# Kernel optimization log

Measured on AMD Instinct MI355X. Metric: run time of the kernel, lower is better.

The kernel has to match this reference:

```python
import jax, jax.numpy as jnp
import numpy as np

NEG_SLOPE = 0.2
EPS = 1e-16


def _add_self_loops(edge_index, num_nodes):
    loop = jnp.arange(num_nodes, dtype=edge_index.dtype)
    return jnp.concatenate([edge_index, jnp.stack([loop, loop])], axis=1)


def gat_conv(x, edge_index, W, a_src, a_dst, b, concat):
    """PyG-style GATConv: gather -> attention logits -> segment softmax -> scatter-add."""
    N = x.shape[0]
    H, C = a_src.shape
    xl = (x @ W).reshape(N, H, C)                       # [N,H,C]
    alpha_src = (xl * a_src[None]).sum(-1)              # [N,H]
    alpha_dst = (xl * a_dst[None]).sum(-1)              # [N,H]
    src, dst = edge_index[0], edge_index[1]
    alpha = jax.nn.leaky_relu(alpha_src[src] + alpha_dst[dst], NEG_SLOPE)  # [E,H]
    amax = jax.ops.segment_max(alpha, dst, num_segments=N)
    amax = jnp.where(jnp.isfinite(amax), amax, 0.0)
    ea = jnp.exp(alpha - amax[dst])
    denom = jax.ops.segment_sum(ea, dst, num_segments=N)
    attn = ea / (denom[dst] + EPS)                      # [E,H]
    msg = xl[src] * attn[:, :, None]                    # [E,H,C]
    out = jax.ops.segment_sum(msg, dst, num_segments=N)  # [N,H,C]
    out = out.reshape(N, H * C) if concat else out.mean(axis=1)
    return out + b


def setup_inputs() -> dict:
    key = jax.random.key(0)
    ks = jax.random.split(key, 9)
    N, F, E, H, C, NC = 100000, 128, 1600000, 8, 8, 40
    s = lambda fan: 1.0 / np.sqrt(fan)
    return {
        "x": jax.random.normal(ks[0], (N, F), dtype=jnp.float32),
        "edge_index": jax.random.randint(ks[1], (2, E), 0, N, dtype=jnp.int64),
        "W1": jax.random.normal(ks[2], (F, H * C), dtype=jnp.float32) * s(F),
        "a_src1": jax.random.normal(ks[3], (H, C), dtype=jnp.float32) * s(C),
        "a_dst1": jax.random.normal(ks[4], (H, C), dtype=jnp.float32) * s(C),
        "b1": jnp.zeros((H * C,), dtype=jnp.float32),
        "W2": jax.random.normal(ks[5], (H * C, NC), dtype=jnp.float32) * s(H * C),
        "a_src2": jax.random.normal(ks[6], (1, NC), dtype=jnp.float32) * s(NC),
        "a_dst2": jax.random.normal(ks[7], (1, NC), dtype=jnp.float32) * s(NC),
        "b2": jnp.zeros((NC,), dtype=jnp.float32),
    }


def reference(x, edge_index, W1, a_src1, a_dst1, b1, W2, a_src2, a_dst2, b2):
    N = x.shape[0]
    ei = _add_self_loops(edge_index, N)
    h = gat_conv(x, ei, W1, a_src1, a_dst1, b1, concat=True)   # [N,64]
    h = jax.nn.elu(h)
    out = gat_conv(h, ei, W2, a_src2, a_dst2, b2, concat=True)  # [N,nclass]
    return out
```

## Files before the change

kernel.cpp:

```cpp
#include <hip/hip_runtime.h>
#include <math.h>

#define NEG_SLOPE 0.2f
#define GAT_EPS 1e-16f

#define CH   8192
#define NBK  256

__device__ __forceinline__ unsigned pack_bf16(float a, float b) {
    unsigned ua = __float_as_uint(a);
    unsigned ub = __float_as_uint(b);
    ua = (ua + 0x8000u) >> 16;
    ub = (ub + 0x8000u) & 0xffff0000u;
    return ua | ub;
}
__device__ __forceinline__ float bf_lo(unsigned pk) {
    return __uint_as_float(pk << 16);
}
__device__ __forceinline__ float bf_hi(unsigned pk) {
    return __uint_as_float(pk & 0xffff0000u);
}


__global__ __launch_bounds__(256) void k_cnt(
    const int* __restrict__ ei, int E, int N, int shift,
    int* __restrict__ cnt)
{
    __shared__ int h[NBK];
    int c = blockIdx.x;
    h[threadIdx.x] = 0;
    __syncthreads();
    int Etot = E + N;
    int base = c * CH;
    int lim = min(base + CH, Etot);
    for (int e = base + threadIdx.x; e < lim; e += 256) {
        int d = (e < E) ? ei[E + e] : (e - E);
        atomicAdd(&h[d >> shift], 1);
    }
    __syncthreads();
    cnt[c * NBK + threadIdx.x] = h[threadIdx.x];
}

__global__ __launch_bounds__(256) void k_off_a(
    const int* __restrict__ cnt, int* __restrict__ off,
    int* __restrict__ tot, int NCH)
{
    __shared__ int sm[256];
    int b = blockIdx.x;
    int t = threadIdx.x;
    int carry = 0;
    for (int c0 = 0; c0 < NCH; c0 += 256) {
        int c = c0 + t;
        int v = (c < NCH) ? cnt[c * NBK + b] : 0;
        sm[t] = v;
        __syncthreads();
        for (int o = 1; o < 256; o <<= 1) {
            int add = (t >= o) ? sm[t - o] : 0;
            __syncthreads();
            sm[t] += add;
            __syncthreads();
        }
        if (c < NCH) off[c * NBK + b] = carry + sm[t] - v;
        carry += sm[255];
        __syncthreads();
    }
    if (t == 0) tot[b] = carry;
}

__global__ __launch_bounds__(256) void k_off_b(
    const int* __restrict__ tot, int* __restrict__ bbase)
{
    __shared__ int sm[NBK];
    int b = threadIdx.x;
    int v0 = tot[b];
    sm[b] = v0;
    __syncthreads();
    for (int o = 1; o < NBK; o <<= 1) {
        int v = (b >= o) ? sm[b - o] : 0;
        __syncthreads();
        sm[b] += v;
        __syncthreads();
    }
    bbase[b] = sm[b] - v0;
    if (b == NBK - 1) bbase[NBK] = sm[b];
}

__global__ __launch_bounds__(256) void k_place(
    const int* __restrict__ ei, int E, int N, int shift,
    const int* __restrict__ off, const int* __restrict__ bbase,
    unsigned* __restrict__ bslab)
{
    __shared__ int cur[NBK];
    int c = blockIdx.x;
    cur[threadIdx.x] = bbase[threadIdx.x] + off[c * NBK + threadIdx.x];
    __syncthreads();
    int Etot = E + N;
    int base = c * CH;
    int lim = min(base + CH, Etot);
    int mask = (1 << shift) - 1;
    for (int e = base + threadIdx.x; e < lim; e += 256) {
        int s, d;
        if (e < E) { s = ei[e]; d = ei[E + e]; }
        else       { s = e - E; d = s; }
        int b = d >> shift;
        int pos = atomicAdd(&cur[b], 1);
        bslab[pos] = (unsigned)s | ((unsigned)(d & mask) << 17);
    }
}

__global__ __launch_bounds__(256) void k_csr2(
    const int* __restrict__ bbase, const unsigned* __restrict__ bslab,
    int shift, int* __restrict__ row_ptr, int* __restrict__ csr_src,
    int N, int Etot)
{
    __shared__ int sdeg[1024];
    __shared__ int scur[1024];
    __shared__ int ps[256];
    int b = blockIdx.x;
    int tid = threadIdx.x;
    int beg = bbase[b], end = bbase[b + 1];
    int nodes = 1 << shift;
    int node0 = b << shift;
    for (int i = tid; i < nodes; i += 256) sdeg[i] = 0;
    __syncthreads();
    for (int i = beg + tid; i < end; i += 256)
        atomicAdd(&sdeg[bslab[i] >> 17], 1);
    __syncthreads();
    int per = (nodes + 255) / 256;
    int mybase = tid * per;
    int sum = 0;
    for (int j = 0; j < per; j++) sum += sdeg[mybase + j];
    ps[tid] = sum;
    __syncthreads();
    int v0 = ps[tid];
    for (int o = 1; o < 256; o <<= 1) {
        int v = (tid >= o) ? ps[tid - o] : 0;
        __syncthreads();
        ps[tid] += v;
        __syncthreads();
    }
    int run = ps[tid] - v0;
    for (int j = 0; j < per; j++) {
        int i = mybase + j;
        int dgi = sdeg[i];
        scur[i] = beg + run;
        int node = node0 + i;
        if (node < N) row_ptr[node] = beg + run;
        run += dgi;
    }
    if (b == 0 && tid == 0) row_ptr[N] = Etot;
    __syncthreads();
    for (int i = beg + tid; i < end; i += 256) {
        unsigned w = bslab[i];
        int pos = atomicAdd(&scur[w >> 17], 1);
        csr_src[pos] = (int)(w & 0x1FFFFu);
    }
}

__global__ __launch_bounds__(256) void k_gemm1(
    const float* __restrict__ x, const float* __restrict__ W1,
    const float* __restrict__ a_src1, const float* __restrict__ a_dst1,
    unsigned* __restrict__ xl1b, float* __restrict__ as1,
    float* __restrict__ ad1, int N, int F)
{
    __shared__ float Ws[128 * 64];
    __shared__ float asrc[64];
    __shared__ float adst[64];
    for (int i = threadIdx.x; i < F * 64; i += 256) Ws[i] = W1[i];
    if (threadIdx.x < 64) {
        asrc[threadIdx.x] = a_src1[threadIdx.x];
        adst[threadIdx.x] = a_dst1[threadIdx.x];
    }
    __syncthreads();

    int n = blockIdx.x * 256 + threadIdx.x;
    if (n >= N) return;

    float acc[64];
#pragma unroll
    for (int c = 0; c < 64; c++) acc[c] = 0.0f;

    const float4* xr4 = (const float4*)(x + (size_t)n * F);
    for (int k4 = 0; k4 < F / 4; k4++) {
        float4 xv = xr4[k4];
        const float* w0 = &Ws[(k4 * 4 + 0) * 64];
        const float* w1 = &Ws[(k4 * 4 + 1) * 64];
        const float* w2 = &Ws[(k4 * 4 + 2) * 64];
        const float* w3 = &Ws[(k4 * 4 + 3) * 64];
#pragma unroll
        for (int c = 0; c < 64; c++) {
            float a = acc[c];
            a = fmaf(xv.x, w0[c], a);
            a = fmaf(xv.y, w1[c], a);
            a = fmaf(xv.z, w2[c], a);
            a = fmaf(xv.w, w3[c], a);
            acc[c] = a;
        }
    }

    unsigned* xo = xl1b + (size_t)n * 32;
#pragma unroll
    for (int p = 0; p < 32; p++) xo[p] = pack_bf16(acc[2 * p], acc[2 * p + 1]);

#pragma unroll
    for (int h = 0; h < 8; h++) {
        float s = 0.0f, t = 0.0f;
#pragma unroll
        for (int c = 0; c < 8; c++) {
            s = fmaf(acc[h * 8 + c], asrc[h * 8 + c], s);
            t = fmaf(acc[h * 8 + c], adst[h * 8 + c], t);
        }
        as1[(size_t)n * 8 + h] = s;
        ad1[(size_t)n * 8 + h] = t;
    }
}

__global__ __launch_bounds__(256) void k_agg1(
    const int* __restrict__ row_ptr, const int* __restrict__ csr_src,
    const float* __restrict__ as1, const float* __restrict__ ad1,
    const unsigned* __restrict__ xl1b, const float* __restrict__ b1,
    float* __restrict__ h1, int N)
{
    int d = blockIdx.x * 4 + (threadIdx.x >> 6);
    int lane = threadIdx.x & 63;
    if (d >= N) return;
    int g = lane >> 3;
    int l = lane & 7;

    int beg = row_ptr[d], end = row_ptr[d + 1];
    float adh = ad1[(size_t)d * 8 + l];

    float ax[8];
#pragma unroll
    for (int j = 0; j < 8; j++) ax[j] = 0.f;
    float den = 0.f;

    for (int i = beg + g; i < end; i += 8) {
        int s = csr_src[i];
        float al = as1[(size_t)s * 8 + l] + adh;
        al = al > 0.f ? al : NEG_SLOPE * al;
        float e = __expf(al);
        uint4 k = *(const uint4*)(xl1b + (size_t)s * 32 + l * 4);
        ax[0] = fmaf(e, bf_lo(k.x), ax[0]);
        ax[1] = fmaf(e, bf_hi(k.x), ax[1]);
        ax[2] = fmaf(e, bf_lo(k.y), ax[2]);
        ax[3] = fmaf(e, bf_hi(k.y), ax[3]);
        ax[4] = fmaf(e, bf_lo(k.z), ax[4]);
        ax[5] = fmaf(e, bf_hi(k.z), ax[5]);
        ax[6] = fmaf(e, bf_lo(k.w), ax[6]);
        ax[7] = fmaf(e, bf_hi(k.w), ax[7]);
        den += e;
    }

#pragma unroll
    for (int m = 8; m < 64; m <<= 1) {
#pragma unroll
        for (int j = 0; j < 8; j++) ax[j] += __shfl_xor(ax[j], m);
        den += __shfl_xor(den, m);
    }

    if (g == 0) {
        float inv = 1.f / (den + GAT_EPS);
        const float4* bb = (const float4*)(b1 + l * 8);
        float4 b0 = bb[0], b1v = bb[1];
        float4 o0, o1;
        float v;
        v = ax[0] * inv + b0.x; o0.x = v > 0.f ? v : expm1f(v);
        v = ax[1] * inv + b0.y; o0.y = v > 0.f ? v : expm1f(v);
        v = ax[2] * inv + b0.z; o0.z = v > 0.f ? v : expm1f(v);
        v = ax[3] * inv + b0.w; o0.w = v > 0.f ? v : expm1f(v);
        v = ax[4] * inv + b1v.x; o1.x = v > 0.f ? v : expm1f(v);
        v = ax[5] * inv + b1v.y; o1.y = v > 0.f ? v : expm1f(v);
        v = ax[6] * inv + b1v.z; o1.z = v > 0.f ? v : expm1f(v);
        v = ax[7] * inv + b1v.w; o1.w = v > 0.f ? v : expm1f(v);
        float4* op = (float4*)(h1 + (size_t)d * 64 + l * 8);
        op[0] = o0;
        op[1] = o1;
    }
}

__global__ __launch_bounds__(256) void k_node2(
    const float* __restrict__ h1, const float* __restrict__ W2,
    const float* __restrict__ a_src2, const float* __restrict__ a_dst2,
    unsigned* __restrict__ xl2b, float* __restrict__ as2,
    float* __restrict__ ad2, int N)
{
    __shared__ float Ws[64 * 40];
    __shared__ float a2s[40];
    __shared__ float a2d[40];
    for (int i = threadIdx.x; i < 64 * 40; i += 256) Ws[i] = W2[i];
    if (threadIdx.x < 40) {
        a2s[threadIdx.x] = a_src2[threadIdx.x];
        a2d[threadIdx.x] = a_dst2[threadIdx.x];
    }
    __syncthreads();

    int n = blockIdx.x * 256 + threadIdx.x;
    if (n >= N) return;

    float o[40];
#pragma unroll
    for (int j = 0; j < 40; j++) o[j] = 0.0f;

    const float* hr = h1 + (size_t)n * 64;
    for (int k = 0; k < 64; k++) {
        float hk = hr[k];
#pragma unroll
        for (int j = 0; j < 40; j++) o[j] = fmaf(hk, Ws[k * 40 + j], o[j]);
    }

    float s = 0.0f, t = 0.0f;
    unsigned* xo = xl2b + (size_t)n * 32;
#pragma unroll
    for (int j = 0; j < 40; j++) {
        s = fmaf(o[j], a2s[j], s);
        t = fmaf(o[j], a2d[j], t);
    }
#pragma unroll
    for (int p = 0; p < 20; p++) xo[p] = pack_bf16(o[2 * p], o[2 * p + 1]);
    as2[n] = s;
    ad2[n] = t;
}

__global__ __launch_bounds__(256) void k_agg2(
    const int* __restrict__ row_ptr, const int* __restrict__ csr_src,
    const float* __restrict__ as2, const float* __restrict__ ad2,
    const unsigned* __restrict__ xl2b, const float* __restrict__ b2,
    float* __restrict__ out, int N)
{
    int d = blockIdx.x * 4 + (threadIdx.x >> 6);
    int lane = threadIdx.x & 63;
    if (d >= N) return;
    int g = lane >> 3;
    int l = lane & 7;

    int beg = row_ptr[d], end = row_ptr[d + 1];
    float add = ad2[d];

    float ax[8];
#pragma unroll
    for (int j = 0; j < 8; j++) ax[j] = 0.f;
    float den = 0.f;

    for (int i = beg + g; i < end; i += 8) {
        int s = csr_src[i];
        float al = as2[s] + add;
        al = al > 0.f ? al : NEG_SLOPE * al;
        float e = __expf(al);
        uint4 k = *(const uint4*)(xl2b + (size_t)s * 32 + l * 4);
        ax[0] = fmaf(e, bf_lo(k.x), ax[0]);
        ax[1] = fmaf(e, bf_hi(k.x), ax[1]);
        ax[2] = fmaf(e, bf_lo(k.y), ax[2]);
        ax[3] = fmaf(e, bf_hi(k.y), ax[3]);
        ax[4] = fmaf(e, bf_lo(k.z), ax[4]);
        ax[5] = fmaf(e, bf_hi(k.z), ax[5]);
        ax[6] = fmaf(e, bf_lo(k.w), ax[6]);
        ax[7] = fmaf(e, bf_hi(k.w), ax[7]);
        den += e;
    }

#pragma unroll
    for (int m = 8; m < 64; m <<= 1) {
#pragma unroll
        for (int j = 0; j < 8; j++) ax[j] += __shfl_xor(ax[j], m);
        den += __shfl_xor(den, m);
    }

    if (g == 0 && l < 5) {
        float inv = 1.f / (den + GAT_EPS);
        float* op = out + (size_t)d * 40 + l * 8;
        const float* bb = b2 + l * 8;
#pragma unroll
        for (int j = 0; j < 8; j++) op[j] = ax[j] * inv + bb[j];
    }
}

extern "C" void kernel_launch(void* const* d_in, const int* in_sizes, int n_in,
                              void* d_out, int out_size, void* d_ws, size_t ws_size,
                              hipStream_t stream) {
    const float* x      = (const float*)d_in[0];
    const int*   ei     = (const int*)d_in[1];
    const float* W1     = (const float*)d_in[2];
    const float* a_src1 = (const float*)d_in[3];
    const float* a_dst1 = (const float*)d_in[4];
    const float* b1     = (const float*)d_in[5];
    const float* W2     = (const float*)d_in[6];
    const float* a_src2 = (const float*)d_in[7];
    const float* a_dst2 = (const float*)d_in[8];
    const float* b2     = (const float*)d_in[9];

    int F = in_sizes[2] / 64;
    int N = in_sizes[0] / F;
    int E = in_sizes[1] / 2;
    int Etot = E + N;
    int NCH = (Etot + CH - 1) / CH;
    int shift = 9;
    while (((N - 1) >> shift) >= NBK) shift++;

    unsigned* xl1b    = (unsigned*)d_ws;
    float*    h1      = (float*)(xl1b + (size_t)N * 32);
    float*    as1     = h1 + (size_t)N * 64;
    float*    ad1     = as1 + (size_t)N * 8;
    int*      row_ptr = (int*)(ad1 + (size_t)N * 8);
    int*      csr_src = row_ptr + (N + 1);
    int*      cnt     = csr_src + Etot;
    int*      off     = cnt + (size_t)NCH * NBK;
    int*      tot     = off + (size_t)NCH * NBK;
    int*      bbase   = tot + NBK;
    unsigned* bslab   = (unsigned*)(bbase + NBK + 1);
    unsigned* xl2b    = xl1b;
    float*    as2     = as1;
    float*    ad2     = ad1;

    k_cnt  <<<NCH, 256, 0, stream>>>(ei, E, N, shift, cnt);
    k_off_a<<<NBK, 256, 0, stream>>>(cnt, off, tot, NCH);
    k_off_b<<<1, 256, 0, stream>>>(tot, bbase);
    k_place<<<NCH, 256, 0, stream>>>(ei, E, N, shift, off, bbase, bslab);
    k_csr2 <<<NBK, 256, 0, stream>>>(bbase, bslab, shift,
                                     row_ptr, csr_src, N, Etot);

    k_gemm1<<<(N + 255) / 256, 256, 0, stream>>>(x, W1, a_src1, a_dst1,
                                                 xl1b, as1, ad1, N, F);
    k_agg1 <<<(N + 3) / 4, 256, 0, stream>>>(row_ptr, csr_src, as1, ad1,
                                             xl1b, b1, h1, N);

    k_node2<<<(N + 255) / 256, 256, 0, stream>>>(h1, W2, a_src2, a_dst2,
                                                 xl2b, as2, ad2, N);
    k_agg2 <<<(N + 3) / 4, 256, 0, stream>>>(row_ptr, csr_src, as2, ad2,
                                             xl2b, b2, (float*)d_out, N);
}
```

Measured before the change: 345.7 us.

## Split node GEMM outputs across multiple threads per node

The first-layer projection kernel now assigns four threads per node, each computing 16 of the 64 output channels, and writes packed bf16 results with vector stores. The second-layer projection uses two threads per node with float4 input loads and a shuffle reduction for the attention scalars. This reduces per-thread register pressure (64 and 40 accumulators down to 16 and 20) and raises the thread count, aiming for better occupancy and latency hiding. In exchange, each x row is loaded redundantly by several threads and more blocks each reload the weight matrix into shared memory.

```diff
diff --git a/kernel.cpp b/kernel.cpp
--- a/kernel.cpp
+++ b/kernel.cpp
@@ -173,22 +173,24 @@
     }
     __syncthreads();
 
-    int n = blockIdx.x * 256 + threadIdx.x;
+    int n = blockIdx.x * 64 + (threadIdx.x >> 2);
+    int q = threadIdx.x & 3;
     if (n >= N) return;
-
-    float acc[64];
-#pragma unroll
-    for (int c = 0; c < 64; c++) acc[c] = 0.0f;
+    int c0 = q * 16;
+
+    float acc[16];
+#pragma unroll
+    for (int c = 0; c < 16; c++) acc[c] = 0.0f;
 
     const float4* xr4 = (const float4*)(x + (size_t)n * F);
     for (int k4 = 0; k4 < F / 4; k4++) {
         float4 xv = xr4[k4];
-        const float* w0 = &Ws[(k4 * 4 + 0) * 64];
-        const float* w1 = &Ws[(k4 * 4 + 1) * 64];
-        const float* w2 = &Ws[(k4 * 4 + 2) * 64];
-        const float* w3 = &Ws[(k4 * 4 + 3) * 64];
-#pragma unroll
-        for (int c = 0; c < 64; c++) {
+        const float* w0 = &Ws[(k4 * 4 + 0) * 64 + c0];
+        const float* w1 = &Ws[(k4 * 4 + 1) * 64 + c0];
+        const float* w2 = &Ws[(k4 * 4 + 2) * 64 + c0];
+        const float* w3 = &Ws[(k4 * 4 + 3) * 64 + c0];
+#pragma unroll
+        for (int c = 0; c < 16; c++) {
             float a = acc[c];
             a = fmaf(xv.x, w0[c], a);
             a = fmaf(xv.y, w1[c], a);
@@ -198,20 +200,25 @@
         }
     }
 
-    unsigned* xo = xl1b + (size_t)n * 32;
-#pragma unroll
-    for (int p = 0; p < 32; p++) xo[p] = pack_bf16(acc[2 * p], acc[2 * p + 1]);
-
-#pragma unroll
-    for (int h = 0; h < 8; h++) {
+    uint4 pk0, pk1;
+    pk0.x = pack_bf16(acc[0], acc[1]);  pk0.y = pack_bf16(acc[2], acc[3]);
+    pk0.z = pack_bf16(acc[4], acc[5]);  pk0.w = pack_bf16(acc[6], acc[7]);
+    pk1.x = pack_bf16(acc[8], acc[9]);  pk1.y = pack_bf16(acc[10], acc[11]);
+    pk1.z = pack_bf16(acc[12], acc[13]); pk1.w = pack_bf16(acc[14], acc[15]);
+    uint4* xo = (uint4*)(xl1b + (size_t)n * 32 + q * 8);
+    xo[0] = pk0;
+    xo[1] = pk1;
+
+#pragma unroll
+    for (int hh = 0; hh < 2; hh++) {
         float s = 0.0f, t = 0.0f;
 #pragma unroll
         for (int c = 0; c < 8; c++) {
-            s = fmaf(acc[h * 8 + c], asrc[h * 8 + c], s);
-            t = fmaf(acc[h * 8 + c], adst[h * 8 + c], t);
+            s = fmaf(acc[hh * 8 + c], asrc[c0 + hh * 8 + c], s);
+            t = fmaf(acc[hh * 8 + c], adst[c0 + hh * 8 + c], t);
         }
-        as1[(size_t)n * 8 + h] = s;
-        ad1[(size_t)n * 8 + h] = t;
+        as1[(size_t)n * 8 + 2 * q + hh] = s;
+        ad1[(size_t)n * 8 + 2 * q + hh] = t;
     }
 }
 
@@ -295,31 +302,46 @@
     }
     __syncthreads();
 
-    int n = blockIdx.x * 256 + threadIdx.x;
+    int n = blockIdx.x * 128 + (threadIdx.x >> 1);
+    int q = threadIdx.x & 1;
     if (n >= N) return;
-
-    float o[40];
-#pragma unroll
-    for (int j = 0; j < 40; j++) o[j] = 0.0f;
-
-    const float* hr = h1 + (size_t)n * 64;
-    for (int k = 0; k < 64; k++) {
-        float hk = hr[k];
-#pragma unroll
-        for (int j = 0; j < 40; j++) o[j] = fmaf(hk, Ws[k * 40 + j], o[j]);
+    int c0 = q * 20;
+
+    float o[20];
+#pragma unroll
+    for (int j = 0; j < 20; j++) o[j] = 0.0f;
+
+    const float4* hr4 = (const float4*)(h1 + (size_t)n * 64);
+    for (int k4 = 0; k4 < 16; k4++) {
+        float4 hv = hr4[k4];
+        const float* w0 = &Ws[(k4 * 4 + 0) * 40 + c0];
+        const float* w1 = &Ws[(k4 * 4 + 1) * 40 + c0];
+        const float* w2 = &Ws[(k4 * 4 + 2) * 40 + c0];
+        const float* w3 = &Ws[(k4 * 4 + 3) * 40 + c0];
+#pragma unroll
+        for (int j = 0; j < 20; j++) {
+            float a = o[j];
+            a = fmaf(hv.x, w0[j], a);
+            a = fmaf(hv.y, w1[j], a);
+            a = fmaf(hv.z, w2[j], a);
+            a = fmaf(hv.w, w3[j], a);
+            o[j] = a;
+        }
     }
 
     float s = 0.0f, t = 0.0f;
-    unsigned* xo = xl2b + (size_t)n * 32;
-#pragma unroll
-    for (int j = 0; j < 40; j++) {
-        s = fmaf(o[j], a2s[j], s);
-        t = fmaf(o[j], a2d[j], t);
-    }
-#pragma unroll
-    for (int p = 0; p < 20; p++) xo[p] = pack_bf16(o[2 * p], o[2 * p + 1]);
-    as2[n] = s;
-    ad2[n] = t;
+#pragma unroll
+    for (int j = 0; j < 20; j++) {
+        s = fmaf(o[j], a2s[c0 + j], s);
+        t = fmaf(o[j], a2d[c0 + j], t);
+    }
+    s += __shfl_xor(s, 1);
+    t += __shfl_xor(t, 1);
+    if (q == 0) { as2[n] = s; ad2[n] = t; }
+
+    unsigned* xo = xl2b + (size_t)n * 32 + q * 10;
+#pragma unroll
+    for (int p = 0; p < 10; p++) xo[p] = pack_bf16(o[2 * p], o[2 * p + 1]);
 }
 
 __global__ __launch_bounds__(256) void k_agg2(
@@ -419,12 +441,12 @@
     k_csr2 <<<NBK, 256, 0, stream>>>(bbase, bslab, shift,
                                      row_ptr, csr_src, N, Etot);
 
-    k_gemm1<<<(N + 255) / 256, 256, 0, stream>>>(x, W1, a_src1, a_dst1,
-                                                 xl1b, as1, ad1, N, F);
+    k_gemm1<<<(N + 63) / 64, 256, 0, stream>>>(x, W1, a_src1, a_dst1,
+                                               xl1b, as1, ad1, N, F);
     k_agg1 <<<(N + 3) / 4, 256, 0, stream>>>(row_ptr, csr_src, as1, ad1,
                                              xl1b, b1, h1, N);
 
-    k_node2<<<(N + 255) / 256, 256, 0, stream>>>(h1, W2, a_src2, a_dst2,
+    k_node2<<<(N + 127) / 128, 256, 0, stream>>>(h1, W2, a_src2, a_dst2,
                                                  xl2b, as2, ad2, N);
     k_agg2 <<<(N + 3) / 4, 256, 0, stream>>>(row_ptr, csr_src, as2, ad2,
                                              xl2b, b2, (float*)d_out, N);
```

Result: faster. 320.8 us (-7.2%).
